# Optimization experiments

Measured on AMD Instinct MI355X. Metric: run time of the kernel, lower is better.

## Reference

```python
import jax, jax.numpy as jnp
import numpy as np
import math

B, T, E, H = 8, 1024, 768, 12
D = E // H  # 64

def setup_inputs() -> dict:
    key = jax.random.key(0)
    ks = jax.random.split(key, 5)
    return {
        "x": jax.random.normal(ks[0], (B, T, E), dtype=jnp.float32),
        "w_attn": jax.random.normal(ks[1], (E, 3 * E), dtype=jnp.float32) * 0.02,
        "b_attn": jax.random.normal(ks[2], (3 * E,), dtype=jnp.float32) * 0.02,
        "w_proj": jax.random.normal(ks[3], (E, E), dtype=jnp.float32) * 0.02,
        "b_proj": jax.random.normal(ks[4], (E,), dtype=jnp.float32) * 0.02,
    }

def reference(x, w_attn, b_attn, w_proj, b_proj):
    b, t, e = x.shape
    h, d = H, E // H
    qkv = x @ w_attn + b_attn                      # [B,T,3E]
    q, k, v = jnp.split(qkv, 3, axis=2)
    q = q.reshape(b, t, h, d).transpose(0, 2, 1, 3)  # [B,H,T,D]
    k = k.reshape(b, t, h, d).transpose(0, 2, 1, 3)
    v = v.reshape(b, t, h, d).transpose(0, 2, 1, 3)
    scores = jnp.einsum('bhqd,bhkd->bhqk', q, k)     # [B,H,T,T]
    causal = jnp.tril(jnp.ones((t, t), dtype=bool))
    scores = jnp.where(causal[None, None], scores, -jnp.inf)
    attn = jax.nn.softmax(scores / jnp.float32(math.sqrt(d)), axis=-1)
    out = jnp.einsum('bhqk,bhkd->bhqd', attn, v)     # [B,H,T,D]
    out = out.transpose(0, 2, 1, 3).reshape(b, t, h * d)
    return out @ w_proj + b_proj
```

## Files before the change

kernel.cpp:

```cpp
#include <hip/hip_runtime.h>
#include <math.h>


#define B_ 8
#define T_ 1024
#define E_ 768
#define H_ 12
#define D_ 64
#define E3 (3 * E_)

typedef __attribute__((ext_vector_type(8))) short bf16x8;
typedef __attribute__((ext_vector_type(4))) float f32x4;

#define SCALE 0.18033688f

__device__ __forceinline__ unsigned short f2bf(float f) {
    unsigned int u = __builtin_bit_cast(unsigned int, f);
    u += 0x7fffu + ((u >> 16) & 1u);
    return (unsigned short)(u >> 16);
}

__device__ __forceinline__ void async_copy16(void* lds, const void* g) {
    __builtin_amdgcn_global_load_lds(
        (const __attribute__((address_space(1))) void*)g,
        (__attribute__((address_space(3))) void*)lds, 16, 0, 0);
}

#define NCVT 6144
#define NTA  (72 * 24)
#define NTP  (24 * 24)

__device__ __forceinline__ void transpose_tile(
    const float* __restrict__ W, unsigned short* __restrict__ Wt,
    int K, int N, int gx, int gy, unsigned short (*tile)[33])
{
    const int n0 = gx * 32, k0 = gy * 32;
    const int tx = threadIdx.x & 31, ty = threadIdx.x >> 5;
    #pragma unroll
    for (int i = 0; i < 4; ++i)
        tile[ty + i * 8][tx] = f2bf(W[(size_t)(k0 + ty + i * 8) * N + n0 + tx]);
    __syncthreads();
    #pragma unroll
    for (int i = 0; i < 4; ++i)
        Wt[(size_t)(n0 + ty + i * 8) * K + k0 + tx] = tile[tx][ty + i * 8];
}

__global__ __launch_bounds__(256) void prep_kernel(
    const float* __restrict__ x, unsigned short* __restrict__ x_bf,
    const float* __restrict__ w_attn, unsigned short* __restrict__ wat,
    const float* __restrict__ w_proj, unsigned short* __restrict__ wpt)
{
    __shared__ unsigned short tile[32][33];
    const int bid = blockIdx.x;
    if (bid < NCVT) {
        const int i = bid * 256 + threadIdx.x;
        float4 f = ((const float4*)x)[i];
        ushort4 o;
        o.x = f2bf(f.x); o.y = f2bf(f.y); o.z = f2bf(f.z); o.w = f2bf(f.w);
        ((ushort4*)x_bf)[i] = o;
    } else if (bid < NCVT + NTA) {
        const int t = bid - NCVT;
        transpose_tile(w_attn, wat, E_, E3, t % 72, t / 72, tile);
    } else {
        const int t = bid - NCVT - NTA;
        transpose_tile(w_proj, wpt, E_, E_, t % 24, t / 24, tile);
    }
}


template <typename OutT, int MODE, int N_>
__global__ __launch_bounds__(256, 2) void gemm_2ph(
    const unsigned short* __restrict__ A,
    const unsigned short* __restrict__ Wt,
    const float* __restrict__ bias,
    OutT* __restrict__ C,
    unsigned short* __restrict__ vt)
{
    constexpr int K = 768;
    constexpr int NKT = 12;
    constexpr int NBX = N_ / 96;
    constexpr int QBX = 768 / 96;
    constexpr int VBX = 1536 / 96;

    extern __shared__ unsigned short lds[];

    const int tid  = threadIdx.x;
    const int lane = tid & 63;
    const int w    = tid >> 6;
    const int wm   = w >> 1;
    const int wn   = w & 1;
    const int n16  = lane & 15;
    const int quad = lane >> 4;

    const int lin = blockIdx.x;
    const int s   = lin >> 3;
    const int by  = (lin & 7) * 8 + s / NBX;
    const int bx  = s % NBX;
    const int bm = by * 128, bn = bx * 96;

    const unsigned short* Asrc = A  + (size_t)bm * K;
    const unsigned short* Bsrc = Wt + (size_t)bn * K;

    auto stage = [&](int bi, int kt) {
        unsigned short* ab = lds + (bi ? 8192 : 0);
        unsigned short* bb = lds + 16384 + (bi ? 6144 : 0);
        #pragma unroll
        for (int i = 0; i < 4; ++i) {
            const int li = i * 256 + tid;
            const int row = li >> 3;
            const int sl  = li & 7;
            async_copy16(&ab[li * 8],
                         Asrc + (size_t)row * K + ((sl ^ (row & 7)) * 8) + kt * 64);
        }
        #pragma unroll
        for (int i = 0; i < 3; ++i) {
            const int li = i * 256 + tid;
            const int row = li >> 3;
            const int sl  = li & 7;
            async_copy16(&bb[li * 8],
                         Bsrc + (size_t)row * K + ((sl ^ (row & 7)) * 8) + kt * 64);
        }
    };

    f32x4 acc[4][3] = {};

#define BARR  __builtin_amdgcn_s_barrier()
#define VM7   asm volatile("s_waitcnt vmcnt(7)" ::: "memory")
#define VM0   asm volatile("s_waitcnt vmcnt(0)" ::: "memory")
#define PRI1  __builtin_amdgcn_s_setprio(1)
#define PRI0  __builtin_amdgcn_s_setprio(0)

    stage(0, 0);

    #pragma unroll 1
    for (int u = 0; u < NKT; ++u) {
        const int bi = u & 1;
        const unsigned short* ab = lds + (bi ? 8192 : 0);
        const unsigned short* bb = lds + 16384 + (bi ? 6144 : 0);
        if (u < NKT - 1) {
            stage(bi ^ 1, u + 1);
            VM7;
        } else {
            VM0;
        }
        BARR;

        #pragma unroll
        for (int kc = 0; kc < 2; ++kc) {
            bf16x8 af[4], bf[3];
            #pragma unroll
            for (int m = 0; m < 4; ++m) {
                const int r = wm * 16 + m * 32 + n16;
                af[m] = *(const bf16x8*)&ab[r * 64 + (((kc * 4 + quad) ^ (r & 7)) * 8)];
            }
            #pragma unroll
            for (int n = 0; n < 3; ++n) {
                const int r = wn * 16 + n * 32 + n16;
                bf[n] = *(const bf16x8*)&bb[r * 64 + (((kc * 4 + quad) ^ (r & 7)) * 8)];
            }
            PRI1;
            #pragma unroll
            for (int m = 0; m < 4; ++m)
                #pragma unroll
                for (int n = 0; n < 3; ++n)
                    acc[m][n] = __builtin_amdgcn_mfma_f32_16x16x32_bf16(
                        af[m], bf[n], acc[m][n], 0, 0, 0);
            PRI0;
        }
        BARR;
    }

#undef VM7
#undef VM0

    if (MODE == 1 && bx >= VBX) {
        #pragma unroll
        for (int m = 0; m < 4; ++m) {
            const int tt = bm + wm * 16 + m * 32 + quad * 4;
            const size_t bb2 = (size_t)(tt >> 10) * 768;
            const int tin = tt & 1023;
            #pragma unroll
            for (int n = 0; n < 3; ++n) {
                const int col = bn + wn * 16 + n * 32 + n16;
                const int ch = col - 1536;
                const float bv = bias[col];
                ushort4 o4;
                o4.x = f2bf(acc[m][n][0] + bv);
                o4.y = f2bf(acc[m][n][1] + bv);
                o4.z = f2bf(acc[m][n][2] + bv);
                o4.w = f2bf(acc[m][n][3] + bv);
                *(ushort4*)&vt[(bb2 + ch) * 1024 + tin] = o4;
            }
        }
        return;
    }

    const bool scale_q = (MODE == 1) && (bx < QBX);
    #pragma unroll
    for (int m = 0; m < 4; ++m) {
        #pragma unroll
        for (int r = 0; r < 4; ++r) {
            const size_t rowoff = (size_t)(bm + wm * 16 + m * 32 + quad * 4 + r) * N_;
            #pragma unroll
            for (int n = 0; n < 3; ++n) {
                const int col = bn + wn * 16 + n * 32 + n16;
                float v = acc[m][n][r] + bias[col];
                if (scale_q) v *= SCALE;
                if constexpr (sizeof(OutT) == 2) C[rowoff + col] = (OutT)f2bf(v);
                else                             C[rowoff + col] = (OutT)v;
            }
        }
    }
}

#define BKEY 128

__global__ __launch_bounds__(256, 3) void flash_attn_kernel(
    const unsigned short* __restrict__ qkv,
    const unsigned short* __restrict__ vt,
    unsigned short* __restrict__ out)
{
    __shared__ __align__(16) unsigned short Ks[2][BKEY * 64];
    __shared__ __align__(16) unsigned short Vts[64 * BKEY];

    const int tid = threadIdx.x;
    const int idx = blockIdx.x;
    const int xcd = idx & 7;
    const int j   = idx >> 3;
    const int head = xcd * 12 + (j % 12);
    const int p    = j / 12;
    const int h = head % H_;
    const int b = head / H_;

    const int lane = tid & 63;
    const int w    = tid >> 6;
    const int n16  = lane & 15;
    const int quad = lane >> 4;

    const size_t base = (size_t)b * T_ * E3;
    const unsigned short* qbase = qkv + base + h * D_;
    const unsigned short* kbase = qkv + base + E_ + h * D_;
    const unsigned short* vtb   = vt + (size_t)(b * H_ + h) * 64 * 1024;

    const int lrow = lane >> 3;
    const int lcol = ((lane & 7) ^ lrow) * 8;
    const int vr4 = lane >> 4;
    const int vc  = lane & 15;

    const int qtA = p, qtB = 15 - p;
    const int nIterA = (qtA + 2) >> 1;
    const int nIterB = (qtB + 2) >> 1;
    const int wqA = qtA * 64 + w * 16;
    const int wqB = qtB * 64 + w * 16;

    const unsigned short* qrpA = qbase + (size_t)(wqA + n16) * E3 + quad * 8;
    bf16x8 qfA0 = *(const bf16x8*)qrpA;
    bf16x8 qfA1 = *(const bf16x8*)(qrpA + 32);
    const unsigned short* qrpB = qbase + (size_t)(wqB + n16) * E3 + quad * 8;
    bf16x8 qfB0 = *(const bf16x8*)qrpB;
    bf16x8 qfB1 = *(const bf16x8*)(qrpB + 32);

    f32x4 oA[4] = {}, oB[4] = {};
    float lsA = 0.f, lsB = 0.f;

    const int sLo = n16 + 32 * (quad & 1);
    const int sHi = sLo + 16;
    const bool hiSel = quad >= 2;

    auto stageK = [&](int t) {
        unsigned short* dst = Ks[t & 1];
        const int k0 = t * BKEY;
        #pragma unroll
        for (int i = 0; i < 4; ++i) {
            const int c = w * 4 + i;
            const int row = c * 8 + lrow;
            async_copy16(&dst[c * 512], kbase + (size_t)(k0 + row) * E3 + lcol);
        }
    };
    auto stageV = [&](int t) {
        const int k0 = t * BKEY;
        #pragma unroll
        for (int i = 0; i < 4; ++i) {
            const int jj = w * 4 + i;
            const int row = 4 * jj + vr4;
            async_copy16(&Vts[4 * jj * BKEY],
                         vtb + (size_t)row * 1024 + k0 + ((vc ^ (row & 15)) * 8));
        }
    };

    auto phase = [&](bf16x8 qf0, bf16x8 qf1, f32x4* o, float& lsum,
                     int wave_q_min, int k0, const unsigned short* Kb,
                     bool doMid, bool notLast) {
        int knt_lim = ((wave_q_min + 15 - k0) >> 4) + 1;
        if (knt_lim > 8) knt_lim = 8;
        const int ks_lim = (knt_lim + 1) >> 1;
        const int nkp = ks_lim * 2;
        int Ab2 = wave_q_min - k0 - 15;
        int kfull = Ab2 < 0 ? 0 : (Ab2 >> 4) + 1;
        if (kfull > 8) kfull = 8;

        const int qcol = wave_q_min + n16;

        f32x4 s[8];
        #pragma unroll
        for (int knt = 0; knt < 8; ++knt) {
            if (knt < knt_lim) {
                const int r = knt * 16 + n16;
                bf16x8 kf0 = *(const bf16x8*)&Kb[r * 64 + ((0 + quad) ^ (r & 7)) * 8];
                bf16x8 kf1 = *(const bf16x8*)&Kb[r * 64 + ((4 + quad) ^ (r & 7)) * 8];
                f32x4 acc = {0.f, 0.f, 0.f, 0.f};
                acc = __builtin_amdgcn_mfma_f32_16x16x32_bf16(kf0, qf0, acc, 0, 0, 0);
                acc = __builtin_amdgcn_mfma_f32_16x16x32_bf16(kf1, qf1, acc, 0, 0, 0);
                s[knt] = acc;
            }
        }
        #pragma unroll
        for (int knt = 0; knt < 8; ++knt) {
            if (knt >= kfull && knt < nkp) {
                const int krow = k0 + knt * 16 + quad * 4;
                #pragma unroll
                for (int r = 0; r < 4; ++r) {
                    float v = (knt < knt_lim) ? s[knt][r] : -1e30f;
                    if (krow + r > qcol) v = -1e30f;
                    s[knt][r] = v;
                }
            }
        }

        unsigned int e0[8], e1[8];
        #pragma unroll
        for (int knt = 0; knt < 8; ++knt) {
            if (knt < nkp) {
                float pv0 = __builtin_amdgcn_exp2f(s[knt][0]);
                float pv1 = __builtin_amdgcn_exp2f(s[knt][1]);
                float pv2 = __builtin_amdgcn_exp2f(s[knt][2]);
                float pv3 = __builtin_amdgcn_exp2f(s[knt][3]);
                lsum += (pv0 + pv1) + (pv2 + pv3);
                unsigned int u0 = __builtin_bit_cast(unsigned int, pv0);
                unsigned int u1 = __builtin_bit_cast(unsigned int, pv1);
                unsigned int u2 = __builtin_bit_cast(unsigned int, pv2);
                unsigned int u3 = __builtin_bit_cast(unsigned int, pv3);
                e0[knt] = ((u0 + 0x8000u) >> 16) | ((u1 + 0x8000u) & 0xffff0000u);
                e1[knt] = ((u2 + 0x8000u) >> 16) | ((u3 + 0x8000u) & 0xffff0000u);
            }
        }

        if (doMid) {
            if (notLast) asm volatile("s_waitcnt vmcnt(4)" ::: "memory");
            else         asm volatile("s_waitcnt vmcnt(0)" ::: "memory");
            __builtin_amdgcn_s_barrier();
        }

        #pragma unroll
        for (int ks = 0; ks < 4; ++ks) {
            if (ks < ks_lim) {
                const int kA = 2 * ks, kB = 2 * ks + 1;
                unsigned int a0 = (unsigned)__shfl((int)e0[kA], sLo);
                unsigned int a1 = (unsigned)__shfl((int)e1[kA], sLo);
                unsigned int a2 = (unsigned)__shfl((int)e0[kA], sHi);
                unsigned int a3 = (unsigned)__shfl((int)e1[kA], sHi);
                unsigned int b0 = (unsigned)__shfl((int)e0[kB], sLo);
                unsigned int b1 = (unsigned)__shfl((int)e1[kB], sLo);
                unsigned int b2 = (unsigned)__shfl((int)e0[kB], sHi);
                unsigned int b3 = (unsigned)__shfl((int)e1[kB], sHi);
                uint4 pu;
                pu.x = hiSel ? b0 : a0;
                pu.y = hiSel ? b1 : a1;
                pu.z = hiSel ? b2 : a2;
                pu.w = hiSel ? b3 : a3;
                bf16x8 pf = __builtin_bit_cast(bf16x8, pu);
                #pragma unroll
                for (int dt = 0; dt < 4; ++dt) {
                    const int row = dt * 16 + n16;
                    bf16x8 vf = *(const bf16x8*)&Vts[row * BKEY +
                                    (((ks * 4 + quad) ^ n16) * 8)];
                    o[dt] = __builtin_amdgcn_mfma_f32_16x16x32_bf16(pf, vf, o[dt], 0, 0, 0);
                }
            }
        }
    };

    stageK(0);
    asm volatile("s_waitcnt vmcnt(0)" ::: "memory");
    __builtin_amdgcn_s_barrier();

    for (int it = 0; it < nIterB; ++it) {
        const int k0 = it * BKEY;
        const bool notLast = (it + 1 < nIterB);

        stageV(it);
        if (notLast) stageK(it + 1);
        const unsigned short* Kb = Ks[it & 1];

        phase(qfB0, qfB1, oB, lsB, wqB, k0, Kb, true,  notLast);
        if (it < nIterA)
            phase(qfA0, qfA1, oA, lsA, wqA, k0, Kb, false, notLast);

        asm volatile("s_waitcnt vmcnt(0)" ::: "memory");
        __builtin_amdgcn_s_barrier();
    }

    lsA += __shfl_xor(lsA, 16); lsA += __shfl_xor(lsA, 32);
    lsB += __shfl_xor(lsB, 16); lsB += __shfl_xor(lsB, 32);

    #pragma unroll
    for (int r = 0; r < 4; ++r) {
        const float invA = 1.f / __shfl(lsA, quad * 4 + r);
        unsigned short* orowA = out + ((size_t)b * T_ + wqA + quad * 4 + r) * E_ + h * D_;
        #pragma unroll
        for (int dt = 0; dt < 4; ++dt)
            orowA[dt * 16 + n16] = f2bf(oA[dt][r] * invA);
        const float invB = 1.f / __shfl(lsB, quad * 4 + r);
        unsigned short* orowB = out + ((size_t)b * T_ + wqB + quad * 4 + r) * E_ + h * D_;
        #pragma unroll
        for (int dt = 0; dt < 4; ++dt)
            orowB[dt * 16 + n16] = f2bf(oB[dt][r] * invB);
    }
}

extern "C" void kernel_launch(void* const* d_in, const int* in_sizes, int n_in,
                              void* d_out, int out_size, void* d_ws, size_t ws_size,
                              hipStream_t stream)
{
    const float* x      = (const float*)d_in[0];
    const float* w_attn = (const float*)d_in[1];
    const float* b_attn = (const float*)d_in[2];
    const float* w_proj = (const float*)d_in[3];
    const float* b_proj = (const float*)d_in[4];
    float* out = (float*)d_out;

    const int M = B_ * T_;

    unsigned short* x_bf   = (unsigned short*)d_ws;
    unsigned short* wat    = x_bf + (size_t)M * E_;
    unsigned short* wpt    = wat + (size_t)E3 * E_;
    unsigned short* qkv_bf = wpt + (size_t)E_ * E_;
    unsigned short* att_bf = qkv_bf + (size_t)M * E3;
    unsigned short* vt_bf  = att_bf + (size_t)M * E_;

    prep_kernel<<<NCVT + NTA + NTP, 256, 0, stream>>>(x, x_bf, w_attn, wat, w_proj, wpt);

    gemm_2ph<unsigned short, 1, E3><<<dim3(1536), dim3(256), 57344, stream>>>(
        x_bf, wat, b_attn, qkv_bf, vt_bf);

    flash_attn_kernel<<<B_ * H_ * 8, 256, 0, stream>>>(qkv_bf, vt_bf, att_bf);

    gemm_2ph<float, 0, E_><<<dim3(512), dim3(256), 57344, stream>>>(
        att_bf, wpt, b_proj, out, nullptr);
}
```

Measured before the change: 174.2 us.

## Retile QKV GEMM to 128x192 with 8 waves and projection to 64x192

Splits the shared templated GEMM into two specialised kernels. The QKV GEMM now uses 128x192 tiles with 512 threads (8 waves in a 2x4 grid) and a per-wave staging layout, which halves the block count and increases B-tile reuse. The projection GEMM uses 64x192 tiles, giving each wave a 2x6 MFMA accumulator block in place of 4x3. Both kernels need more dynamic LDS, set through hipFuncSetAttribute, and the larger LDS footprint may reduce how many blocks fit on each CU.

Result: faster. 170.1 us (-2.3%).

```diff
diff --git a/kernel.cpp b/kernel.cpp
--- a/kernel.cpp
+++ b/kernel.cpp
@@ -67,65 +67,58 @@
     }
 }
 
-
-template <typename OutT, int MODE, int N_>
-__global__ __launch_bounds__(256, 2) void gemm_2ph(
+__global__ __launch_bounds__(512, 4) void gemm_qkv_128x192(
     const unsigned short* __restrict__ A,
     const unsigned short* __restrict__ Wt,
     const float* __restrict__ bias,
-    OutT* __restrict__ C,
+    unsigned short* __restrict__ C,
     unsigned short* __restrict__ vt)
 {
     constexpr int K = 768;
+    constexpr int N = E3;
     constexpr int NKT = 12;
-    constexpr int NBX = N_ / 96;
-    constexpr int QBX = 768 / 96;
-    constexpr int VBX = 1536 / 96;
 
     extern __shared__ unsigned short lds[];
 
     const int tid  = threadIdx.x;
     const int lane = tid & 63;
     const int w    = tid >> 6;
-    const int wm   = w >> 1;
-    const int wn   = w & 1;
+    const int wm   = w >> 2;
+    const int wn   = w & 3;
     const int n16  = lane & 15;
     const int quad = lane >> 4;
-
-    const int lin = blockIdx.x;
-    const int s   = lin >> 3;
-    const int by  = (lin & 7) * 8 + s / NBX;
-    const int bx  = s % NBX;
-    const int bm = by * 128, bn = bx * 96;
-
-    const unsigned short* Asrc = A  + (size_t)bm * K;
-    const unsigned short* Bsrc = Wt + (size_t)bn * K;
+    const int l7   = lane & 7;
+    const int lrow = lane >> 3;
+    const int lcol = (l7 ^ lrow) * 8;
+
+    const int lin  = blockIdx.x;
+    const int s    = lin >> 3;
+    const int by   = (lin & 7) * 8 + s / 12;
+    const int bx   = s % 12;
+    const int bm = by * 128, bn = bx * 192;
+
+    const unsigned short* Asrc = A  + (size_t)(bm + lrow) * K + lcol;
+    const unsigned short* Bsrc = Wt + (size_t)(bn + lrow) * K + lcol;
 
     auto stage = [&](int bi, int kt) {
         unsigned short* ab = lds + (bi ? 8192 : 0);
-        unsigned short* bb = lds + 16384 + (bi ? 6144 : 0);
-        #pragma unroll
-        for (int i = 0; i < 4; ++i) {
-            const int li = i * 256 + tid;
-            const int row = li >> 3;
-            const int sl  = li & 7;
-            async_copy16(&ab[li * 8],
-                         Asrc + (size_t)row * K + ((sl ^ (row & 7)) * 8) + kt * 64);
+        unsigned short* bb = lds + 16384 + (bi ? 12288 : 0);
+        #pragma unroll
+        for (int i = 0; i < 2; ++i) {
+            const int c = w * 2 + i;
+            async_copy16(&ab[c * 512], Asrc + (size_t)(c * 8) * K + kt * 64);
         }
         #pragma unroll
         for (int i = 0; i < 3; ++i) {
-            const int li = i * 256 + tid;
-            const int row = li >> 3;
-            const int sl  = li & 7;
-            async_copy16(&bb[li * 8],
-                         Bsrc + (size_t)row * K + ((sl ^ (row & 7)) * 8) + kt * 64);
+            const int c = w * 3 + i;
+            async_copy16(&bb[c * 512], Bsrc + (size_t)(c * 8) * K + kt * 64);
         }
     };
 
     f32x4 acc[4][3] = {};
 
 #define BARR  __builtin_amdgcn_s_barrier()
-#define VM7   asm volatile("s_waitcnt vmcnt(7)" ::: "memory")
+#define VM5   asm volatile("s_waitcnt vmcnt(5)" ::: "memory")
 #define VM0   asm volatile("s_waitcnt vmcnt(0)" ::: "memory")
 #define PRI1  __builtin_amdgcn_s_setprio(1)
 #define PRI0  __builtin_amdgcn_s_setprio(0)
@@ -136,10 +129,10 @@
     for (int u = 0; u < NKT; ++u) {
         const int bi = u & 1;
         const unsigned short* ab = lds + (bi ? 8192 : 0);
-        const unsigned short* bb = lds + 16384 + (bi ? 6144 : 0);
+        const unsigned short* bb = lds + 16384 + (bi ? 12288 : 0);
         if (u < NKT - 1) {
             stage(bi ^ 1, u + 1);
-            VM7;
+            VM5;
         } else {
             VM0;
         }
@@ -155,7 +148,7 @@
             }
             #pragma unroll
             for (int n = 0; n < 3; ++n) {
-                const int r = wn * 16 + n * 32 + n16;
+                const int r = wn * 16 + n * 64 + n16;
                 bf[n] = *(const bf16x8*)&bb[r * 64 + (((kc * 4 + quad) ^ (r & 7)) * 8)];
             }
             PRI1;
@@ -170,10 +163,10 @@
         BARR;
     }
 
-#undef VM7
+#undef VM5
 #undef VM0
 
-    if (MODE == 1 && bx >= VBX) {
+    if (bx >= 8) {
         #pragma unroll
         for (int m = 0; m < 4; ++m) {
             const int tt = bm + wm * 16 + m * 32 + quad * 4;
@@ -181,7 +174,7 @@
             const int tin = tt & 1023;
             #pragma unroll
             for (int n = 0; n < 3; ++n) {
-                const int col = bn + wn * 16 + n * 32 + n16;
+                const int col = bn + wn * 16 + n * 64 + n16;
                 const int ch = col - 1536;
                 const float bv = bias[col];
                 ushort4 o4;
@@ -192,22 +185,134 @@
                 *(ushort4*)&vt[(bb2 + ch) * 1024 + tin] = o4;
             }
         }
-        return;
-    }
-
-    const bool scale_q = (MODE == 1) && (bx < QBX);
+    } else {
+        const bool scale_q = bx < 4;
+        #pragma unroll
+        for (int m = 0; m < 4; ++m) {
+            #pragma unroll
+            for (int r = 0; r < 4; ++r) {
+                const size_t rowoff = (size_t)(bm + wm * 16 + m * 32 + quad * 4 + r) * N;
+                #pragma unroll
+                for (int n = 0; n < 3; ++n) {
+                    const int col = bn + wn * 16 + n * 64 + n16;
+                    float v = acc[m][n][r] + bias[col];
+                    if (scale_q) v *= SCALE;
+                    C[rowoff + col] = f2bf(v);
+                }
+            }
+        }
+    }
+}
+
+__global__ __launch_bounds__(256, 2) void gemm_proj_64x192(
+    const unsigned short* __restrict__ A,
+    const unsigned short* __restrict__ Wt,
+    const float* __restrict__ bias,
+    float* __restrict__ C)
+{
+    constexpr int K = 768;
+    constexpr int NKT = 12;
+
+    extern __shared__ unsigned short lds[];
+
+    const int tid  = threadIdx.x;
+    const int lane = tid & 63;
+    const int w    = tid >> 6;
+    const int wm   = w >> 1;
+    const int wn   = w & 1;
+    const int n16  = lane & 15;
+    const int quad = lane >> 4;
+
+    const int lin = blockIdx.x;
+    const int s   = lin >> 3;
+    const int by  = (lin & 7) * 16 + (s >> 2);
+    const int bx  = s & 3;
+    const int bm = by * 64, bn = bx * 192;
+
+    const unsigned short* Asrc = A  + (size_t)bm * K;
+    const unsigned short* Bsrc = Wt + (size_t)bn * K;
+
+    auto stage = [&](int bi, int kt) {
+        unsigned short* ab = lds + (bi ? 4096 : 0);
+        unsigned short* bb = lds + 8192 + (bi ? 12288 : 0);
+        #pragma unroll
+        for (int i = 0; i < 2; ++i) {
+            const int li = i * 256 + tid;
+            const int row = li >> 3;
+            const int sl  = li & 7;
+            async_copy16(&ab[li * 8],
+                         Asrc + (size_t)row * K + ((sl ^ (row & 7)) * 8) + kt * 64);
+        }
+        #pragma unroll
+        for (int i = 0; i < 6; ++i) {
+            const int li = i * 256 + tid;
+            const int row = li >> 3;
+            const int sl  = li & 7;
+            async_copy16(&bb[li * 8],
+                         Bsrc + (size_t)row * K + ((sl ^ (row & 7)) * 8) + kt * 64);
+        }
+    };
+
+    f32x4 acc[2][6] = {};
+
+#define BARR  __builtin_amdgcn_s_barrier()
+#define VM8   asm volatile("s_waitcnt vmcnt(8)" ::: "memory")
+#define VM0   asm volatile("s_waitcnt vmcnt(0)" ::: "memory")
+#define PRI1  __builtin_amdgcn_s_setprio(1)
+#define PRI0  __builtin_amdgcn_s_setprio(0)
+
+    stage(0, 0);
+
+    #pragma unroll 1
+    for (int u = 0; u < NKT; ++u) {
+        const int bi = u & 1;
+        const unsigned short* ab = lds + (bi ? 4096 : 0);
+        const unsigned short* bb = lds + 8192 + (bi ? 12288 : 0);
+        if (u < NKT - 1) {
+            stage(bi ^ 1, u + 1);
+            VM8;
+        } else {
+            VM0;
+        }
+        BARR;
+
+        #pragma unroll
+        for (int kc = 0; kc < 2; ++kc) {
+            bf16x8 af[2], bf[6];
+            #pragma unroll
+            for (int m = 0; m < 2; ++m) {
+                const int r = wm * 16 + m * 32 + n16;
+                af[m] = *(const bf16x8*)&ab[r * 64 + (((kc * 4 + quad) ^ (r & 7)) * 8)];
+            }
+            #pragma unroll
+            for (int n = 0; n < 6; ++n) {
+                const int r = wn * 16 + n * 32 + n16;
+                bf[n] = *(const bf16x8*)&bb[r * 64 + (((kc * 4 + quad) ^ (r & 7)) * 8)];
+            }
+            PRI1;
+            #pragma unroll
+            for (int m = 0; m < 2; ++m)
+                #pragma unroll
+                for (int n = 0; n < 6; ++n)
+                    acc[m][n] = __builtin_amdgcn_mfma_f32_16x16x32_bf16(
+                        af[m], bf[n], acc[m][n], 0, 0, 0);
+            PRI0;
+        }
+        BARR;
+    }
+
+#undef VM8
+#undef VM0
+
     #pragma unroll
-    for (int m = 0; m < 4; ++m) {
+    for (int m = 0; m < 2; ++m) {
         #pragma unroll
         for (int r = 0; r < 4; ++r) {
-            const size_t rowoff = (size_t)(bm + wm * 16 + m * 32 + quad * 4 + r) * N_;
-            #pragma unroll
-            for (int n = 0; n < 3; ++n) {
+            const size_t rowoff = (size_t)(bm + wm * 16 + m * 32 + quad * 4 + r) * E_;
+            #pragma unroll
+            for (int n = 0; n < 6; ++n) {
                 const int col = bn + wn * 16 + n * 32 + n16;
-                float v = acc[m][n][r] + bias[col];
-                if (scale_q) v *= SCALE;
-                if constexpr (sizeof(OutT) == 2) C[rowoff + col] = (OutT)f2bf(v);
-                else                             C[rowoff + col] = (OutT)v;
+                C[rowoff + col] = acc[m][n][r] + bias[col];
             }
         }
     }
@@ -438,13 +543,22 @@
     unsigned short* att_bf = qkv_bf + (size_t)M * E3;
     unsigned short* vt_bf  = att_bf + (size_t)M * E_;
 
+    static bool attr_set = false;
+    if (!attr_set) {
+        (void)hipFuncSetAttribute((const void*)gemm_qkv_128x192,
+                                  hipFuncAttributeMaxDynamicSharedMemorySize, 81920);
+        (void)hipFuncSetAttribute((const void*)gemm_proj_64x192,
+                                  hipFuncAttributeMaxDynamicSharedMemorySize, 65536);
+        attr_set = true;
+    }
+
     prep_kernel<<<NCVT + NTA + NTP, 256, 0, stream>>>(x, x_bf, w_attn, wat, w_proj, wpt);
 
-    gemm_2ph<unsigned short, 1, E3><<<dim3(1536), dim3(256), 57344, stream>>>(
+    gemm_qkv_128x192<<<dim3(768), dim3(512), 81920, stream>>>(
         x_bf, wat, b_attn, qkv_bf, vt_bf);
 
     flash_attn_kernel<<<B_ * H_ * 8, 256, 0, stream>>>(qkv_bf, vt_bf, att_bf);
 
-    gemm_2ph<float, 0, E_><<<dim3(512), dim3(256), 57344, stream>>>(
-        att_bf, wpt, b_proj, out, nullptr);
-}
+    gemm_proj_64x192<<<dim3(512), dim3(256), 65536, stream>>>(
+        att_bf, wpt, b_proj, out);
+}
```
